# Kernel tuning notes

Measured on AMD Instinct MI355X. Metric: run time of the kernel, lower is better.

Reference implementation:

```python
import jax, jax.numpy as jnp
import numpy as np

THETA = 10000.0
AXES_DIM = (16, 56, 56)  # sums to head_dim=128
HEADS = 24
HEAD_DIM = 128
EPS = 1e-5


def _pos_embed(ids):
    # ids: (S, n_axes) int -> cos, sin each (S, head_dim//2)
    pos = ids.astype(jnp.float32)
    cos_out, sin_out = [], []
    for i, d in enumerate(AXES_DIM):
        freqs = 1.0 / (THETA ** (jnp.arange(0, d, 2, dtype=jnp.float32) / d))  # (d/2,)
        ang = pos[:, i][:, None] * freqs[None, :]  # (S, d/2)
        cos_out.append(jnp.cos(ang))
        sin_out.append(jnp.sin(ang))
    return jnp.concatenate(cos_out, -1), jnp.concatenate(sin_out, -1)


def _rms_norm(x, w):
    # per-head RMSNorm over last dim (head_dim)
    var = jnp.mean(x * x, axis=-1, keepdims=True)
    return x * jax.lax.rsqrt(var + EPS) * w


def _apply_rope(x, cos, sin):
    # non-neox (interleaved) rotary. x: (B,S,H,D), cos/sin: (S,D/2)
    x1 = x[..., 0::2]
    x2 = x[..., 1::2]
    c = cos[None, :, None, :]
    s = sin[None, :, None, :]
    o1 = x1 * c - x2 * s
    o2 = x2 * c + x1 * s
    return jnp.stack([o1, o2], axis=-1).reshape(x.shape)


def setup_inputs() -> dict:
    key = jax.random.key(0)
    ks = jax.random.split(key, 12)
    B, S_img, S_txt, D = 1, 2048, 512, 3072
    sd = 1.0 / np.sqrt(D)
    return {
        "hidden_states": jax.random.normal(ks[0], (B, S_img, D), jnp.float32),
        "encoder_hidden_states": jax.random.normal(ks[1], (B, S_txt, D), jnp.float32),
        "ids": jax.random.randint(ks[2], (S_txt + S_img, 3), 0, 64, jnp.int32),
        "w_qkv": jax.random.normal(ks[3], (D, 3 * D), jnp.float32) * sd,
        "w_add_qkv": jax.random.normal(ks[4], (D, 3 * D), jnp.float32) * sd,
        "b_add_qkv": jax.random.normal(ks[5], (3 * D,), jnp.float32) * 0.02,
        "w_out": jax.random.normal(ks[6], (D, D), jnp.float32) * sd,
        "b_out": jax.random.normal(ks[7], (D,), jnp.float32) * 0.02,
        "w_add_out": jax.random.normal(ks[8], (D, D), jnp.float32) * sd,
        "b_add_out": jax.random.normal(ks[9], (D,), jnp.float32) * 0.02,
        "norm_q_w": jnp.ones((HEAD_DIM,), jnp.float32),
        "norm_k_w": jnp.ones((HEAD_DIM,), jnp.float32),
        "norm_add_q_w": jnp.ones((HEAD_DIM,), jnp.float32),
        "norm_add_k_w": jnp.ones((HEAD_DIM,), jnp.float32),
    }


def reference(hidden_states, encoder_hidden_states, ids, w_qkv, w_add_qkv,
              b_add_qkv, w_out, b_out, w_add_out, b_add_out,
              norm_q_w, norm_k_w, norm_add_q_w, norm_add_k_w):
    B, S_img, D = hidden_states.shape
    S_txt = encoder_hidden_states.shape[1]
    H, Dh = HEADS, HEAD_DIM

    # fused QKV projections
    qkv = hidden_states @ w_qkv  # (B, S_img, 3D)
    q, k, v = jnp.split(qkv, 3, axis=-1)
    q = _rms_norm(q.reshape(B, S_img, H, Dh), norm_q_w)
    k = _rms_norm(k.reshape(B, S_img, H, Dh), norm_k_w)
    v = v.reshape(B, S_img, H, Dh)

    eqkv = encoder_hidden_states @ w_add_qkv + b_add_qkv
    eq, ek, ev = jnp.split(eqkv, 3, axis=-1)
    eq = _rms_norm(eq.reshape(B, S_txt, H, Dh), norm_add_q_w)
    ek = _rms_norm(ek.reshape(B, S_txt, H, Dh), norm_add_k_w)
    ev = ev.reshape(B, S_txt, H, Dh)

    # joint sequence: text first, then image
    q = jnp.concatenate([eq, q], axis=1)
    k = jnp.concatenate([ek, k], axis=1)
    v = jnp.concatenate([ev, v], axis=1)

    # multi-axis RoPE over joint positions
    cos, sin = _pos_embed(ids)  # (S_txt+S_img, Dh/2)
    q = _apply_rope(q, cos, sin)
    k = _apply_rope(k, cos, sin)

    # scaled dot-product attention (non-causal)
    scale = 1.0 / np.sqrt(Dh)
    scores = jnp.einsum("bqhd,bkhd->bhqk", q, k) * scale
    probs = jax.nn.softmax(scores, axis=-1)
    attn = jnp.einsum("bhqk,bkhd->bqhd", probs, v)
    attn = attn.reshape(B, S_txt + S_img, H * Dh)

    enc_out = attn[:, :S_txt] @ w_add_out + b_add_out
    img_out = attn[:, S_txt:] @ w_out + b_out
    return img_out, enc_out
```

## Files before the change

### kernel.cpp

```cpp
#include <hip/hip_runtime.h>

typedef __attribute__((ext_vector_type(8))) short short8;
typedef __attribute__((ext_vector_type(4))) short short4v;
typedef __attribute__((ext_vector_type(4))) float floatx4;

__device__ __forceinline__ float b2f(short b) {
  union { unsigned u; float f; } v; v.u = ((unsigned)(unsigned short)b) << 16; return v.f;
}
__device__ __forceinline__ short f2b(float f) {
  union { float f; unsigned u; } v; v.f = f;
  return (short)((v.u + 0x7fffu + ((v.u >> 16) & 1u)) >> 16);
}
__device__ __forceinline__ unsigned cvtpk(float lo, float hi) {
  unsigned r;
  asm("v_cvt_pk_bf16_f32 %0, %1, %2" : "=v"(r) : "v"(lo), "v"(hi));
  return r;
}
__device__ __forceinline__ float loadf(const void* p, size_t i, bool f32) {
  return f32 ? ((const float*)p)[i] : b2f(((const short*)p)[i]);
}
__device__ __forceinline__ short8 load8(const void* p, size_t i, bool f32) {
  if (f32) {
    const float* fp = (const float*)p + i;
    float4 a = *(const float4*)fp;
    float4 b = *(const float4*)(fp + 4);
    short8 r;
    r[0] = f2b(a.x); r[1] = f2b(a.y); r[2] = f2b(a.z); r[3] = f2b(a.w);
    r[4] = f2b(b.x); r[5] = f2b(b.y); r[6] = f2b(b.z); r[7] = f2b(b.w);
    return r;
  }
  return *(const short8*)((const short*)p + i);
}

__device__ __forceinline__ void gload16(const short* g, short* l) {
  __builtin_amdgcn_global_load_lds(
      (const __attribute__((address_space(1))) unsigned int*)g,
      (__attribute__((address_space(3))) unsigned int*)l, 16, 0, 0);
}

__global__ void detect_dtype(const unsigned short* __restrict__ w, int* __restrict__ flag) {
  __shared__ int cnt;
  if (threadIdx.x == 0) cnt = 0;
  __syncthreads();
  int bad = 0;
  for (int i = threadIdx.x; i < 4096; i += 256) {
    int e = (w[i] >> 7) & 0xFF;
    if (e >= 0xC8) bad++;
  }
  atomicAdd(&cnt, bad);
  __syncthreads();
  if (threadIdx.x == 0) *flag = (cnt > 64) ? 1 : 0;
}

__global__ __launch_bounds__(256)
void cvt_bf16_2(const void* __restrict__ srcA, long n8A,
                const void* __restrict__ srcB, long n8B,
                short* __restrict__ dst, const int* __restrict__ dflag) {
  const bool f32 = (*dflag != 0);
  const long n8 = n8A + n8B;
  long stride = (long)gridDim.x * 256;
  for (long i = (long)blockIdx.x * 256 + threadIdx.x; i < n8; i += stride) {
    const void* s; long e;
    if (i < n8A) { s = srcA; e = i * 8; } else { s = srcB; e = (i - n8A) * 8; }
    if (f32) {
      const float* fp = (const float*)s + e;
      float4 a = *(const float4*)fp;
      float4 b = *(const float4*)(fp + 4);
      short8 r;
      r[0] = f2b(a.x); r[1] = f2b(a.y); r[2] = f2b(a.z); r[3] = f2b(a.w);
      r[4] = f2b(b.x); r[5] = f2b(b.y); r[6] = f2b(b.z); r[7] = f2b(b.w);
      *(short8*)(dst + i * 8) = r;
    } else {
      *(short8*)(dst + i * 8) = *(const short8*)((const short*)s + e);
    }
  }
}

__global__ __launch_bounds__(256)
void cvt_tw(const void* __restrict__ wq, short* __restrict__ wqd,
            const void* __restrict__ waq, short* __restrict__ waqd,
            const void* __restrict__ wo, short* __restrict__ wod,
            const void* __restrict__ wao, short* __restrict__ waod,
            const int* __restrict__ dflag) {
  __shared__ short st[64][72];
  const bool f32 = (*dflag != 0);
  const int K = 3072;
  int b = blockIdx.x;
  const void* src; short* dst; int N, n0, k0;
  if (b < 13824) {
    src = (b < 6912) ? wq : waq;
    dst = (b < 6912) ? wqd : waqd;
    int rem = b % 6912;
    N = 9216; n0 = (rem % 144) << 6; k0 = (rem / 144) << 6;
  } else {
    b -= 13824;
    src = (b < 2304) ? wo : wao;
    dst = (b < 2304) ? wod : waod;
    int rem = b % 2304;
    N = 3072; n0 = (rem % 48) << 6; k0 = (rem / 48) << 6;
  }
  const int c4 = threadIdx.x & 15;
  const int rq = threadIdx.x >> 4;
#pragma unroll
  for (int r = 0; r < 4; ++r) {
    int k = r * 16 + rq;
    int n = c4 * 4;
    short v0, v1, v2, v3;
    if (f32) {
      const float* sp = (const float*)src + (size_t)(k0 + k) * N + n0 + n;
      float4 f = *(const float4*)sp;
      v0 = f2b(f.x); v1 = f2b(f.y); v2 = f2b(f.z); v3 = f2b(f.w);
    } else {
      const short* sp = (const short*)src + (size_t)(k0 + k) * N + n0 + n;
      short4v s = *(const short4v*)sp;
      v0 = s[0]; v1 = s[1]; v2 = s[2]; v3 = s[3];
    }
    st[n + 0][k] = v0; st[n + 1][k] = v1; st[n + 2][k] = v2; st[n + 3][k] = v3;
  }
  __syncthreads();
  const int n = threadIdx.x >> 2;
  const int kc = (threadIdx.x & 3) << 4;
  short8 a = *(const short8*)(&st[n][kc]);
  short8 bb = *(const short8*)(&st[n][kc + 8]);
  short* dp = dst + (size_t)(n0 + n) * K + k0 + kc;
  *(short8*)(dp) = a;
  *(short8*)(dp + 8) = bb;
}

__global__ __launch_bounds__(256, 2)
void gemm_bt(const void* __restrict__ A, int a_row0,
             const void* __restrict__ B, const void* __restrict__ bias,
             void* __restrict__ C, int c_row0, int N, int K,
             const int* __restrict__ dflag, int aIn, int cOut) {
  __shared__ short As[128 * 32];
  __shared__ short Bs[128 * 32];
  const bool f32 = (*dflag != 0);
  const bool a32 = aIn && f32;
  const bool c32 = cOut && f32;
  const int tid = threadIdx.x;
  const int lane = tid & 63, w = tid >> 6;
  const int wm = w & 1, wn = w >> 1;
  const int qg = lane >> 4, l16 = lane & 15;
  const int m0 = blockIdx.y << 7, n0 = blockIdx.x << 7;

  const int arow = tid >> 2, ak = (tid & 3) << 3;
  const int brow = tid >> 4, bc = (tid & 15) << 3;
  const int rot = tid & 15;

  floatx4 acc[4][4];
#pragma unroll
  for (int i = 0; i < 4; ++i)
#pragma unroll
    for (int j = 0; j < 4; ++j) acc[i][j] = (floatx4){0.f, 0.f, 0.f, 0.f};

  for (int k0 = 0; k0 < K; k0 += 32) {
    __syncthreads();
#pragma unroll
    for (int j = 0; j < 2; ++j) {
      short8 av = load8(A, (size_t)(a_row0 + m0 + j * 64 + arow) * K + (k0 + ak), a32);
      *(short8*)(As + (j * 64 + arow) * 32 + ak) = av;
      int kr = j * 16 + brow;
      short8 bv = load8(B, (size_t)(k0 + kr) * N + (n0 + bc), f32);
      int kq = kr >> 3, kj = kr & 7;
#pragma unroll
      for (int s = 0; s < 8; ++s) {
        int u = (s + rot) & 7;
        int n = bc + u;
        Bs[(n << 5) + ((kq ^ (n & 3)) << 3) + kj] = bv[u];
      }
    }
    __syncthreads();
    short8 a[4];
#pragma unroll
    for (int mi = 0; mi < 4; ++mi)
      a[mi] = *(const short8*)(As + (wm * 64 + mi * 16 + l16) * 32 + qg * 8);
#pragma unroll
    for (int ni = 0; ni < 4; ++ni) {
      int n = wn * 64 + ni * 16 + l16;
      short8 b = *(const short8*)(Bs + (n << 5) + ((qg ^ (n & 3)) << 3));
#pragma unroll
      for (int mi = 0; mi < 4; ++mi)
        acc[mi][ni] = __builtin_amdgcn_mfma_f32_16x16x32_bf16(a[mi], b, acc[mi][ni], 0, 0, 0);
    }
  }
#pragma unroll
  for (int ni = 0; ni < 4; ++ni) {
    int col = n0 + wn * 64 + ni * 16 + l16;
    float bv = bias ? loadf(bias, col, f32) : 0.0f;
#pragma unroll
    for (int mi = 0; mi < 4; ++mi) {
      int row = m0 + wm * 64 + mi * 16 + qg * 4;
#pragma unroll
      for (int r = 0; r < 4; ++r) {
        size_t idx = (size_t)(c_row0 + row + r) * N + col;
        float val = acc[mi][ni][r] + bv;
        if (c32) ((float*)C)[idx] = val;
        else     ((short*)C)[idx] = f2b(val);
      }
    }
  }
}

__global__ __launch_bounds__(256, 3)
void gemm_bf2(const short* __restrict__ A,
              const short* __restrict__ BTa, const void* __restrict__ biasa,
              int a0a, int c0a, int nYa,
              const short* __restrict__ BTb, const void* __restrict__ biasb,
              int a0b, int c0b,
              void* __restrict__ C, int N, int K,
              const int* __restrict__ dflag, int cOut) {
  __shared__ short Ls[6 * 128 * 32];
#define ASB(b) (Ls + (b) * 4096)
#define BSB(b) (Ls + (3 + (b)) * 4096)
  const bool f32 = (*dflag != 0);
  const bool c32 = cOut && f32;
  const int bx = blockIdx.x;
  const int y = blockIdx.y;
  const short* BT; const void* bias; int arow0, crow0;
  if (y < nYa) { BT = BTa; bias = biasa; arow0 = a0a + (y << 7); crow0 = c0a + (y << 7); }
  else { int my = y - nYa; BT = BTb; bias = biasb; arow0 = a0b + (my << 7); crow0 = c0b + (my << 7); }
  const int tid = threadIdx.x;
  const int lane = tid & 63, w = tid >> 6;
  const int wm = w & 1, wn = w >> 1;
  const int qg = lane >> 4, l16 = lane & 15;
  const int n0 = bx << 7;
  const int garow = lane >> 2;
  const int gcir = lane & 3;
  const int nk = K >> 5;
  const int swz = (gcir ^ (garow & 3) ^ (garow >> 2)) << 3;
  const short* Abase = A + (size_t)(arow0 + w * 32 + garow) * K + swz;
  const short* Bbase = BT + (size_t)(n0 + w * 32 + garow) * K + swz;
  const int rswz = (l16 & 3) ^ (l16 >> 2);

  floatx4 acc[4][4];
#pragma unroll
  for (int i = 0; i < 4; ++i)
#pragma unroll
    for (int j = 0; j < 4; ++j) acc[i][j] = (floatx4){0.f, 0.f, 0.f, 0.f};

  auto STAGE = [&](int buf, int k0) {
#pragma unroll
    for (int j = 0; j < 2; ++j) {
      gload16(Abase + (size_t)j * 16 * K + k0, ASB(buf) + ((w * 2 + j) << 9));
      gload16(Bbase + (size_t)j * 16 * K + k0, BSB(buf) + ((w * 2 + j) << 9));
    }
  };

  STAGE(0, 0);
  if (nk > 1) STAGE(1, 32);

  int cb = 0;
  for (int t = 0; t < nk; ++t) {
    if (t + 1 < nk) {
      asm volatile("s_waitcnt vmcnt(4) lgkmcnt(0)" ::: "memory");
    } else {
      asm volatile("s_waitcnt vmcnt(0) lgkmcnt(0)" ::: "memory");
    }
    __builtin_amdgcn_s_barrier();
    if (t + 2 < nk) {
      int sb = (cb == 0) ? 2 : cb - 1;
      STAGE(sb, (t + 2) << 5);
    }
    short8 a[4], b[4];
#pragma unroll
    for (int mi = 0; mi < 4; ++mi) {
      int ra = wm * 64 + mi * 16 + l16;
      a[mi] = *(const short8*)(ASB(cb) + (ra << 5) + ((qg ^ rswz) << 3));
    }
#pragma unroll
    for (int ni = 0; ni < 4; ++ni) {
      int n = wn * 64 + ni * 16 + l16;
      b[ni] = *(const short8*)(BSB(cb) + (n << 5) + ((qg ^ rswz) << 3));
    }
    __builtin_amdgcn_s_setprio(1);
#pragma unroll
    for (int ni = 0; ni < 4; ++ni)
#pragma unroll
      for (int mi = 0; mi < 4; ++mi)
        acc[mi][ni] = __builtin_amdgcn_mfma_f32_16x16x32_bf16(a[mi], b[ni], acc[mi][ni], 0, 0, 0);
    __builtin_amdgcn_s_setprio(0);
    cb = (cb == 2) ? 0 : cb + 1;
  }
  __builtin_amdgcn_s_barrier();
  if (!c32) {
    short* wreg = Ls + w * 4096;
#pragma unroll
    for (int ni = 0; ni < 4; ++ni) {
      float bvv = bias ? loadf(bias, n0 + wn * 64 + ni * 16 + l16, f32) : 0.0f;
#pragma unroll
      for (int mi = 0; mi < 4; ++mi)
#pragma unroll
        for (int r = 0; r < 4; ++r)
          wreg[(mi * 16 + qg * 4 + r) * 64 + ni * 16 + l16] = f2b(acc[mi][ni][r] + bvv);
    }
    asm volatile("s_waitcnt lgkmcnt(0)" ::: "memory");
#pragma unroll
    for (int j = 0; j < 8; ++j) {
      int row = j * 8 + (lane >> 3);
      int col = (lane & 7) * 8;
      short8 v = *(const short8*)(wreg + row * 64 + col);
      *(short8*)((short*)C + (size_t)(crow0 + wm * 64 + row) * N + n0 + wn * 64 + col) = v;
    }
  } else {
    float* wregf = (float*)(Ls) + w * 2048;
#pragma unroll
    for (int half = 0; half < 2; ++half) {
#pragma unroll
      for (int nh = 0; nh < 2; ++nh) {
        int ni = half * 2 + nh;
        float bvv = bias ? loadf(bias, n0 + wn * 64 + ni * 16 + l16, f32) : 0.0f;
#pragma unroll
        for (int mi = 0; mi < 4; ++mi)
#pragma unroll
          for (int r = 0; r < 4; ++r)
            wregf[(mi * 16 + qg * 4 + r) * 32 + nh * 16 + l16] = acc[mi][ni][r] + bvv;
      }
      asm volatile("s_waitcnt lgkmcnt(0)" ::: "memory");
#pragma unroll
      for (int j = 0; j < 8; ++j) {
        int row = j * 8 + (lane >> 3);
        int c4 = (lane & 7) * 4;
        float4 v = *(const float4*)(wregf + row * 32 + c4);
        *(float4*)((float*)C + (size_t)(crow0 + wm * 64 + row) * N + n0 + wn * 64 + half * 32 + c4) = v;
      }
      asm volatile("s_waitcnt lgkmcnt(0)" ::: "memory");
    }
  }
#undef ASB
#undef BSB
}

__global__ __launch_bounds__(512)
void norm_rope(short* __restrict__ qkv, const int* __restrict__ ids,
               const void* __restrict__ nqw, const void* __restrict__ nkw,
               const void* __restrict__ naqw, const void* __restrict__ nakw,
               const int* __restrict__ dflag) {
  const bool f32 = (*dflag != 0);
  const int t = blockIdx.x, wv = threadIdx.x >> 6, lane = threadIdx.x & 63;
  const bool txt = t < 512;
  int p = lane, axis; float expo;
  if (p < 8)       { axis = 0; expo = (float)(2 * p) * (1.0f / 16.0f); }
  else if (p < 36) { axis = 1; expo = (float)(2 * (p - 8)) * (1.0f / 56.0f); }
  else             { axis = 2; expo = (float)(2 * (p - 36)) * (1.0f / 56.0f); }
  float freq = __expf(-expo * 9.210340371976184f);
  float ang = (float)ids[t * 3 + axis] * freq;
  float s, c; sincosf(ang, &s, &c);
  const void* qw = txt ? naqw : nqw;
  const void* kw = txt ? nakw : nkw;
  float w0q = loadf(qw, 2 * lane, f32), w1q = loadf(qw, 2 * lane + 1, f32);
  float w0k = loadf(kw, 2 * lane, f32), w1k = loadf(kw, 2 * lane + 1, f32);
  const float QS = 0.08838834764831845f * 1.4426950408889634f;
#pragma unroll
  for (int i = 0; i < 3; ++i) {
    int h = wv + 8 * i;
    short* qp = qkv + (size_t)t * 9216 + h * 128 + 2 * lane;
    short* kp = qp + 3072;
    union { unsigned u; short sh[2]; } qv, kv;
    qv.u = *(const unsigned*)qp;
    kv.u = *(const unsigned*)kp;
    float q0 = b2f(qv.sh[0]), q1 = b2f(qv.sh[1]);
    float k0 = b2f(kv.sh[0]), k1 = b2f(kv.sh[1]);
    float sq = q0 * q0 + q1 * q1, sk = k0 * k0 + k1 * k1;
#pragma unroll
    for (int o = 1; o < 64; o <<= 1) { sq += __shfl_xor(sq, o); sk += __shfl_xor(sk, o); }
    float rq = rsqrtf(sq * (1.0f / 128.0f) + 1e-5f);
    float rk = rsqrtf(sk * (1.0f / 128.0f) + 1e-5f);
    float qn0 = q0 * rq * w0q, qn1 = q1 * rq * w1q;
    float kn0 = k0 * rk * w0k, kn1 = k1 * rk * w1k;
    float qo0 = qn0 * c - qn1 * s, qo1 = qn1 * c + qn0 * s;
    float ko0 = kn0 * c - kn1 * s, ko1 = kn1 * c + kn0 * s;
    union { unsigned u; short sh[2]; } qo, ko;
    qo.sh[0] = f2b(qo0 * QS);
    qo.sh[1] = f2b(qo1 * QS);
    ko.sh[0] = f2b(ko0); ko.sh[1] = f2b(ko1);
    *(unsigned*)qp = qo.u;
    *(unsigned*)kp = ko.u;
  }
}

__global__ __launch_bounds__(512, 2)
void attn_fa(const short* __restrict__ qkv, short* __restrict__ attn) {
  __shared__ short QPs[256 * 128];
  __shared__ short KVs[2][128 * 128];
  const int wgid = blockIdx.x;
  const int xcd = wgid & 7, slot = wgid >> 3;
  const int h = xcd * 3 + slot / 10;
  const int qt = slot % 10;
  const int tid = threadIdx.x, lane = tid & 63, w = tid >> 6;
  const int qg = lane >> 4, l16 = lane & 15;
  const int lr = lane >> 4, lc = lane & 15;
  const int q0 = qt << 8;
  const int sc = tid & 15;
  const int srow5 = (tid >> 4) & 15, half = tid >> 8;

  const short* Qg  = qkv + (size_t)q0 * 9216 + h * 128;
  const short* Kg0 = qkv + 3072 + h * 128;
  const short* Vg0 = qkv + 6144 + h * 128;

  short8 vr[4];
#pragma unroll
  for (int j = 0; j < 8; ++j) {
    int row = j * 32 + w * 4 + lr;
    gload16(Qg + (size_t)row * 9216 + ((lc ^ (row & 7)) << 3),
            QPs + (j * 32 + w * 4) * 128);
  }
#pragma unroll
  for (int j = 0; j < 4; ++j) {
    int row = j * 32 + w * 4 + lr;
    gload16(Kg0 + (size_t)row * 9216 + ((lc ^ (row & 7)) << 3),
            &KVs[0][(j * 32 + w * 4) * 128]);
  }
#pragma unroll
  for (int j = 0; j < 4; ++j) {
    int row = half * 64 + j * 16 + srow5;
    vr[j] = *(const short8*)(Vg0 + (size_t)row * 9216 + sc * 8);
  }
  asm volatile("s_waitcnt vmcnt(8) lgkmcnt(0)" ::: "memory");
  __builtin_amdgcn_s_barrier();
  short8 aq[2][4];
#pragma unroll
  for (int mi = 0; mi < 2; ++mi)
#pragma unroll
    for (int kc = 0; kc < 4; ++kc) {
      int row = w * 32 + mi * 16 + l16;
      aq[mi][kc] = *(const short8*)(QPs + row * 128 + (((kc * 4 + qg) ^ (row & 7)) << 3));
    }

  floatx4 acc_o[2][8];
#pragma unroll
  for (int mi = 0; mi < 2; ++mi)
#pragma unroll
    for (int nd = 0; nd < 8; ++nd) acc_o[mi][nd] = (floatx4){0.f, 0.f, 0.f, 0.f};
  float m_i[2][4], l_i[2][4];
#pragma unroll
  for (int mi = 0; mi < 2; ++mi)
#pragma unroll
    for (int r = 0; r < 4; ++r) { m_i[mi][r] = -1e30f; l_i[mi][r] = 0.0f; }

  for (int kt = 0; kt < 20; ++kt) {
    const int c = kt & 1;
    asm volatile("s_waitcnt vmcnt(4) lgkmcnt(0)" ::: "memory");
    __builtin_amdgcn_s_barrier();
    if (kt < 19) {
      const short* Kg = qkv + ((size_t)(kt + 1) * 128) * 9216 + 3072 + h * 128;
#pragma unroll
      for (int j = 0; j < 4; ++j) {
        int row = j * 32 + w * 4 + lr;
        gload16(Kg + (size_t)row * 9216 + ((lc ^ (row & 7)) << 3),
                &KVs[1 - c][(j * 32 + w * 4) * 128]);
      }
    }
    floatx4 acc_s[2][8];
#pragma unroll
    for (int mi = 0; mi < 2; ++mi)
#pragma unroll
      for (int ni = 0; ni < 8; ++ni) acc_s[mi][ni] = (floatx4){0.f, 0.f, 0.f, 0.f};
    __builtin_amdgcn_s_setprio(1);
#pragma unroll
    for (int kc = 0; kc < 4; ++kc) {
#pragma unroll
      for (int ni = 0; ni < 8; ++ni) {
        int row = ni * 16 + l16;
        short8 b = *(const short8*)(&KVs[c][row * 128 + (((kc * 4 + qg) ^ (row & 7)) << 3)]);
        acc_s[0][ni] = __builtin_amdgcn_mfma_f32_16x16x32_bf16(aq[0][kc], b, acc_s[0][ni], 0, 0, 0);
        acc_s[1][ni] = __builtin_amdgcn_mfma_f32_16x16x32_bf16(aq[1][kc], b, acc_s[1][ni], 0, 0, 0);
      }
    }
    __builtin_amdgcn_s_setprio(0);
    float mxv[2][4];
    bool need = false;
#pragma unroll
    for (int mi = 0; mi < 2; ++mi) {
#pragma unroll
      for (int r = 0; r < 4; ++r) {
        float mx = acc_s[mi][0][r];
#pragma unroll
        for (int ni = 1; ni < 8; ++ni) mx = fmaxf(mx, acc_s[mi][ni][r]);
        mx = fmaxf(mx, __shfl_xor(mx, 1));
        mx = fmaxf(mx, __shfl_xor(mx, 2));
        mx = fmaxf(mx, __shfl_xor(mx, 4));
        mx = fmaxf(mx, __shfl_xor(mx, 8));
        mxv[mi][r] = mx;
        need = need || (mx > m_i[mi][r] + 8.0f);
      }
    }
    if (__ballot(need)) {
#pragma unroll
      for (int mi = 0; mi < 2; ++mi) {
#pragma unroll
        for (int r = 0; r < 4; ++r) {
          float mn = fmaxf(m_i[mi][r], mxv[mi][r]);
          float al = __builtin_amdgcn_exp2f(m_i[mi][r] - mn);
          m_i[mi][r] = mn;
          l_i[mi][r] *= al;
#pragma unroll
          for (int nd = 0; nd < 8; ++nd) acc_o[mi][nd][r] *= al;
        }
      }
    }
#pragma unroll
    for (int mi = 0; mi < 2; ++mi) {
      float rs[4] = {0.f, 0.f, 0.f, 0.f};
#pragma unroll
      for (int r = 0; r < 4; ++r) {
        float pv[8];
#pragma unroll
        for (int ni = 0; ni < 8; ++ni) {
          pv[ni] = __builtin_amdgcn_exp2f(acc_s[mi][ni][r] - m_i[mi][r]);
          rs[r] += pv[ni];
        }
        unsigned u0 = cvtpk(pv[0], pv[1]);
        unsigned u1 = cvtpk(pv[2], pv[3]);
        unsigned u2 = cvtpk(pv[4], pv[5]);
        unsigned u3 = cvtpk(pv[6], pv[7]);
        int row = w * 32 + mi * 16 + qg * 4 + r;
        uint4 uu; uu.x = u0; uu.y = u1; uu.z = u2; uu.w = u3;
        *(uint4*)(QPs + row * 128 + ((l16 ^ (row & 15)) << 3)) = uu;
      }
#pragma unroll
      for (int r = 0; r < 4; ++r) {
        float t = rs[r];
        t += __shfl_xor(t, 1); t += __shfl_xor(t, 2);
        t += __shfl_xor(t, 4); t += __shfl_xor(t, 8);
        l_i[mi][r] += t;
      }
    }
    asm volatile("s_waitcnt lgkmcnt(0)" ::: "memory");
    __builtin_amdgcn_s_barrier();
#pragma unroll
    for (int u = 0; u < 8; ++u) {
      int d = sc * 8 + u;
      short4v pk = { vr[0][u], vr[1][u], vr[2][u], vr[3][u] };
      *(short4v*)(&KVs[c][d * 128 + (((srow5 ^ u ^ (sc & 7))) << 3) + half * 4]) = pk;
    }
    if (kt < 19) {
      const short* Vg = qkv + ((size_t)(kt + 1) * 128) * 9216 + 6144 + h * 128;
#pragma unroll
      for (int j = 0; j < 4; ++j) {
        int row = half * 64 + j * 16 + srow5;
        vr[j] = *(const short8*)(Vg + (size_t)row * 9216 + sc * 8);
      }
    }
    asm volatile("s_waitcnt lgkmcnt(0)" ::: "memory");
    __builtin_amdgcn_s_barrier();
    __builtin_amdgcn_s_setprio(1);
#pragma unroll
    for (int kc = 0; kc < 4; ++kc) {
      int prow0 = w * 32 + l16;
      short8 ap0 = *(const short8*)(QPs + prow0 * 128 + (((kc * 4 + qg) ^ (prow0 & 15)) << 3));
      int prow1 = prow0 + 16;
      short8 ap1 = *(const short8*)(QPs + prow1 * 128 + (((kc * 4 + qg) ^ (prow1 & 15)) << 3));
#pragma unroll
      for (int nd = 0; nd < 8; ++nd) {
        int row = nd * 16 + l16;
        int chn = (kc * 4 + qg) ^ (row & 7) ^ ((row >> 3) & 7);
        short8 b = *(const short8*)(&KVs[c][row * 128 + (chn << 3)]);
        acc_o[0][nd] = __builtin_amdgcn_mfma_f32_16x16x32_bf16(ap0, b, acc_o[0][nd], 0, 0, 0);
        acc_o[1][nd] = __builtin_amdgcn_mfma_f32_16x16x32_bf16(ap1, b, acc_o[1][nd], 0, 0, 0);
      }
    }
    __builtin_amdgcn_s_setprio(0);
  }
#pragma unroll
  for (int mi = 0; mi < 2; ++mi) {
    float inv[4];
#pragma unroll
    for (int r = 0; r < 4; ++r) inv[r] = 1.0f / l_i[mi][r];
#pragma unroll
    for (int nd = 0; nd < 8; ++nd) {
#pragma unroll
      for (int r = 0; r < 4; ++r) {
        int row = w * 32 + mi * 16 + qg * 4 + r;
        QPs[row * 128 + nd * 16 + l16] = f2b(acc_o[mi][nd][r] * inv[r]);
      }
    }
  }
  asm volatile("s_waitcnt lgkmcnt(0)" ::: "memory");
#pragma unroll
  for (int j = 0; j < 8; ++j) {
    int rrow = w * 32 + j * 4 + qg;
    short8 vv = *(const short8*)(QPs + rrow * 128 + l16 * 8);
    *(short8*)(attn + (size_t)(q0 + rrow) * 3072 + h * 128 + l16 * 8) = vv;
  }
}

extern "C" void kernel_launch(void* const* d_in, const int* in_sizes, int n_in,
                              void* d_out, int out_size, void* d_ws, size_t ws_size,
                              hipStream_t stream) {
  (void)in_sizes; (void)n_in; (void)out_size;
  const void* hidden    = d_in[0];
  const void* enc       = d_in[1];
  const int*  ids       = (const int*)d_in[2];
  const void* w_qkv     = d_in[3];
  const void* w_add_qkv = d_in[4];
  const void* b_add_qkv = d_in[5];
  const void* w_out     = d_in[6];
  const void* b_out     = d_in[7];
  const void* w_add_out = d_in[8];
  const void* b_add_out = d_in[9];
  const void* nqw  = d_in[10];
  const void* nkw  = d_in[11];
  const void* naqw = d_in[12];
  const void* nakw = d_in[13];

  int*   dflag = (int*)d_ws;
  short* qkv   = (short*)((char*)d_ws + 256);
  short* attnB = qkv + (size_t)2560 * 9216;

  short* pool  = attnB + (size_t)2560 * 3072;
  const long n_hid  = 2048L * 3072;
  const long n_enc  = 512L * 3072;
  const long n_wqkv = 3072L * 9216;
  const long n_wout = 3072L * 3072;
  short* xb   = pool;
  short* wqb  = xb + n_enc + n_hid;
  short* waqb = wqb + n_wqkv;
  short* wob  = waqb + n_wqkv;
  short* waob = wob + n_wout;
  const size_t REQ = 256 + 2 * ((size_t)2560 * 9216 + (size_t)2560 * 3072 +
                                n_hid + n_enc + 2 * n_wqkv + 2 * n_wout);

  detect_dtype<<<1, 256, 0, stream>>>((const unsigned short*)w_qkv, dflag);

  if (ws_size >= REQ) {
    cvt_bf16_2<<<1024, 256, 0, stream>>>(enc, n_enc / 8, hidden, n_hid / 8, xb, dflag);
    cvt_tw<<<dim3(18432), 256, 0, stream>>>(w_qkv, wqb, w_add_qkv, waqb,
                                            w_out, wob, w_add_out, waob, dflag);

    gemm_bf2<<<dim3(72, 20), 256, 0, stream>>>(
        xb, waqb, b_add_qkv, 0, 0, 4, wqb, nullptr, 512, 512,
        qkv, 9216, 3072, dflag, 0);
    norm_rope<<<dim3(2560), 512, 0, stream>>>(qkv, ids, nqw, nkw, naqw, nakw, dflag);
    attn_fa<<<dim3(240), 512, 0, stream>>>(qkv, attnB);
    gemm_bf2<<<dim3(24, 20), 256, 0, stream>>>(
        attnB, wob, b_out, 512, 0, 16, waob, b_add_out, 0, 2048,
        d_out, 3072, 3072, dflag, 1);
  } else {
    gemm_bt<<<dim3(72, 4), 256, 0, stream>>>(enc, 0, w_add_qkv, b_add_qkv, qkv, 0, 9216, 3072, dflag, 1, 0);
    gemm_bt<<<dim3(72, 16), 256, 0, stream>>>(hidden, 0, w_qkv, nullptr, qkv, 512, 9216, 3072, dflag, 1, 0);
    norm_rope<<<dim3(2560), 512, 0, stream>>>(qkv, ids, nqw, nkw, naqw, nakw, dflag);
    attn_fa<<<dim3(240), 512, 0, stream>>>(qkv, attnB);
    gemm_bt<<<dim3(24, 16), 256, 0, stream>>>(attnB, 512, w_out, b_out, d_out, 0, 3072, 3072, dflag, 0, 1);
    gemm_bt<<<dim3(24, 4), 256, 0, stream>>>(attnB, 0, w_add_out, b_add_out, d_out, 2048, 3072, 3072, dflag, 0, 1);
  }
}
```

Baseline: 792.4 us.

## Enlarge GEMM block tile to 256x128 with 8x4 MFMA per wave

Doubles the M dimension of the gemm_bf2 block tile from 128 to 256 rows, so each wave computes a 128x64 sub-tile with twice the accumulators. Each B tile loaded into shared memory now feeds twice as many MFMAs, which cuts global and LDS traffic per FLOP, and the grid shrinks by half. The cost is more registers and shared memory per block (launch bounds lowered to 2 blocks per CU) and fewer blocks: the output projection drops to 240 blocks, which may not fill all CUs.

After: 792.9 us. No clear change (+0.1%).

```diff
diff --git a/kernel.cpp b/kernel.cpp
--- a/kernel.cpp
+++ b/kernel.cpp
@@ -201,7 +201,7 @@
   }
 }
 
-__global__ __launch_bounds__(256, 3)
+__global__ __launch_bounds__(256, 2)
 void gemm_bf2(const short* __restrict__ A,
               const short* __restrict__ BTa, const void* __restrict__ biasa,
               int a0a, int c0a, int nYa,
@@ -209,16 +209,16 @@
               int a0b, int c0b,
               void* __restrict__ C, int N, int K,
               const int* __restrict__ dflag, int cOut) {
-  __shared__ short Ls[6 * 128 * 32];
-#define ASB(b) (Ls + (b) * 4096)
-#define BSB(b) (Ls + (3 + (b)) * 4096)
+  __shared__ short Ls[3 * 8192 + 3 * 4096];
+#define ASB(b) (Ls + (b) * 8192)
+#define BSB(b) (Ls + 24576 + (b) * 4096)
   const bool f32 = (*dflag != 0);
   const bool c32 = cOut && f32;
   const int bx = blockIdx.x;
   const int y = blockIdx.y;
   const short* BT; const void* bias; int arow0, crow0;
-  if (y < nYa) { BT = BTa; bias = biasa; arow0 = a0a + (y << 7); crow0 = c0a + (y << 7); }
-  else { int my = y - nYa; BT = BTb; bias = biasb; arow0 = a0b + (my << 7); crow0 = c0b + (my << 7); }
+  if (y < nYa) { BT = BTa; bias = biasa; arow0 = a0a + (y << 8); crow0 = c0a + (y << 8); }
+  else { int my = y - nYa; BT = BTb; bias = biasb; arow0 = a0b + (my << 8); crow0 = c0b + (my << 8); }
   const int tid = threadIdx.x;
   const int lane = tid & 63, w = tid >> 6;
   const int wm = w & 1, wn = w >> 1;
@@ -228,22 +228,23 @@
   const int gcir = lane & 3;
   const int nk = K >> 5;
   const int swz = (gcir ^ (garow & 3) ^ (garow >> 2)) << 3;
-  const short* Abase = A + (size_t)(arow0 + w * 32 + garow) * K + swz;
+  const short* Abase = A + (size_t)(arow0 + w * 64 + garow) * K + swz;
   const short* Bbase = BT + (size_t)(n0 + w * 32 + garow) * K + swz;
   const int rswz = (l16 & 3) ^ (l16 >> 2);
 
-  floatx4 acc[4][4];
-#pragma unroll
-  for (int i = 0; i < 4; ++i)
+  floatx4 acc[8][4];
+#pragma unroll
+  for (int i = 0; i < 8; ++i)
 #pragma unroll
     for (int j = 0; j < 4; ++j) acc[i][j] = (floatx4){0.f, 0.f, 0.f, 0.f};
 
   auto STAGE = [&](int buf, int k0) {
 #pragma unroll
-    for (int j = 0; j < 2; ++j) {
-      gload16(Abase + (size_t)j * 16 * K + k0, ASB(buf) + ((w * 2 + j) << 9));
+    for (int j = 0; j < 4; ++j)
+      gload16(Abase + (size_t)j * 16 * K + k0, ASB(buf) + ((w * 4 + j) << 9));
+#pragma unroll
+    for (int j = 0; j < 2; ++j)
       gload16(Bbase + (size_t)j * 16 * K + k0, BSB(buf) + ((w * 2 + j) << 9));
-    }
   };
 
   STAGE(0, 0);
@@ -252,7 +253,7 @@
   int cb = 0;
   for (int t = 0; t < nk; ++t) {
     if (t + 1 < nk) {
-      asm volatile("s_waitcnt vmcnt(4) lgkmcnt(0)" ::: "memory");
+      asm volatile("s_waitcnt vmcnt(6) lgkmcnt(0)" ::: "memory");
     } else {
       asm volatile("s_waitcnt vmcnt(0) lgkmcnt(0)" ::: "memory");
     }
@@ -261,10 +262,10 @@
       int sb = (cb == 0) ? 2 : cb - 1;
       STAGE(sb, (t + 2) << 5);
     }
-    short8 a[4], b[4];
-#pragma unroll
-    for (int mi = 0; mi < 4; ++mi) {
-      int ra = wm * 64 + mi * 16 + l16;
+    short8 a[8], b[4];
+#pragma unroll
+    for (int mi = 0; mi < 8; ++mi) {
+      int ra = wm * 128 + mi * 16 + l16;
       a[mi] = *(const short8*)(ASB(cb) + (ra << 5) + ((qg ^ rswz) << 3));
     }
 #pragma unroll
@@ -276,7 +277,7 @@
 #pragma unroll
     for (int ni = 0; ni < 4; ++ni)
 #pragma unroll
-      for (int mi = 0; mi < 4; ++mi)
+      for (int mi = 0; mi < 8; ++mi)
         acc[mi][ni] = __builtin_amdgcn_mfma_f32_16x16x32_bf16(a[mi], b[ni], acc[mi][ni], 0, 0, 0);
     __builtin_amdgcn_s_setprio(0);
     cb = (cb == 2) ? 0 : cb + 1;
@@ -285,45 +286,56 @@
   if (!c32) {
     short* wreg = Ls + w * 4096;
 #pragma unroll
-    for (int ni = 0; ni < 4; ++ni) {
-      float bvv = bias ? loadf(bias, n0 + wn * 64 + ni * 16 + l16, f32) : 0.0f;
-#pragma unroll
-      for (int mi = 0; mi < 4; ++mi)
-#pragma unroll
-        for (int r = 0; r < 4; ++r)
-          wreg[(mi * 16 + qg * 4 + r) * 64 + ni * 16 + l16] = f2b(acc[mi][ni][r] + bvv);
-    }
-    asm volatile("s_waitcnt lgkmcnt(0)" ::: "memory");
-#pragma unroll
-    for (int j = 0; j < 8; ++j) {
-      int row = j * 8 + (lane >> 3);
-      int col = (lane & 7) * 8;
-      short8 v = *(const short8*)(wreg + row * 64 + col);
-      *(short8*)((short*)C + (size_t)(crow0 + wm * 64 + row) * N + n0 + wn * 64 + col) = v;
+    for (int half = 0; half < 2; ++half) {
+#pragma unroll
+      for (int ni = 0; ni < 4; ++ni) {
+        float bvv = bias ? loadf(bias, n0 + wn * 64 + ni * 16 + l16, f32) : 0.0f;
+#pragma unroll
+        for (int mi2 = 0; mi2 < 4; ++mi2)
+#pragma unroll
+          for (int r = 0; r < 4; ++r)
+            wreg[(mi2 * 16 + qg * 4 + r) * 64 + ni * 16 + l16] =
+                f2b(acc[half * 4 + mi2][ni][r] + bvv);
+      }
+      asm volatile("s_waitcnt lgkmcnt(0)" ::: "memory");
+#pragma unroll
+      for (int j = 0; j < 8; ++j) {
+        int row = j * 8 + (lane >> 3);
+        int col = (lane & 7) * 8;
+        short8 v = *(const short8*)(wreg + row * 64 + col);
+        *(short8*)((short*)C + (size_t)(crow0 + wm * 128 + half * 64 + row) * N +
+                   n0 + wn * 64 + col) = v;
+      }
+      asm volatile("s_waitcnt lgkmcnt(0)" ::: "memory");
     }
   } else {
     float* wregf = (float*)(Ls) + w * 2048;
 #pragma unroll
     for (int half = 0; half < 2; ++half) {
 #pragma unroll
-      for (int nh = 0; nh < 2; ++nh) {
-        int ni = half * 2 + nh;
-        float bvv = bias ? loadf(bias, n0 + wn * 64 + ni * 16 + l16, f32) : 0.0f;
-#pragma unroll
-        for (int mi = 0; mi < 4; ++mi)
-#pragma unroll
-          for (int r = 0; r < 4; ++r)
-            wregf[(mi * 16 + qg * 4 + r) * 32 + nh * 16 + l16] = acc[mi][ni][r] + bvv;
-      }
-      asm volatile("s_waitcnt lgkmcnt(0)" ::: "memory");
-#pragma unroll
-      for (int j = 0; j < 8; ++j) {
-        int row = j * 8 + (lane >> 3);
-        int c4 = (lane & 7) * 4;
-        float4 v = *(const float4*)(wregf + row * 32 + c4);
-        *(float4*)((float*)C + (size_t)(crow0 + wm * 64 + row) * N + n0 + wn * 64 + half * 32 + c4) = v;
-      }
-      asm volatile("s_waitcnt lgkmcnt(0)" ::: "memory");
+      for (int ch = 0; ch < 2; ++ch) {
+#pragma unroll
+        for (int nh = 0; nh < 2; ++nh) {
+          int ni = ch * 2 + nh;
+          float bvv = bias ? loadf(bias, n0 + wn * 64 + ni * 16 + l16, f32) : 0.0f;
+#pragma unroll
+          for (int mi2 = 0; mi2 < 4; ++mi2)
+#pragma unroll
+            for (int r = 0; r < 4; ++r)
+              wregf[(mi2 * 16 + qg * 4 + r) * 32 + nh * 16 + l16] =
+                  acc[half * 4 + mi2][ni][r] + bvv;
+        }
+        asm volatile("s_waitcnt lgkmcnt(0)" ::: "memory");
+#pragma unroll
+        for (int j = 0; j < 8; ++j) {
+          int row = j * 8 + (lane >> 3);
+          int c4 = (lane & 7) * 4;
+          float4 v = *(const float4*)(wregf + row * 32 + c4);
+          *(float4*)((float*)C + (size_t)(crow0 + wm * 128 + half * 64 + row) * N +
+                     n0 + wn * 64 + ch * 32 + c4) = v;
+        }
+        asm volatile("s_waitcnt lgkmcnt(0)" ::: "memory");
+      }
     }
   }
 #undef ASB
@@ -627,13 +639,13 @@
     cvt_tw<<<dim3(18432), 256, 0, stream>>>(w_qkv, wqb, w_add_qkv, waqb,
                                             w_out, wob, w_add_out, waob, dflag);
 
-    gemm_bf2<<<dim3(72, 20), 256, 0, stream>>>(
-        xb, waqb, b_add_qkv, 0, 0, 4, wqb, nullptr, 512, 512,
+    gemm_bf2<<<dim3(72, 10), 256, 0, stream>>>(
+        xb, waqb, b_add_qkv, 0, 0, 2, wqb, nullptr, 512, 512,
         qkv, 9216, 3072, dflag, 0);
     norm_rope<<<dim3(2560), 512, 0, stream>>>(qkv, ids, nqw, nkw, naqw, nakw, dflag);
     attn_fa<<<dim3(240), 512, 0, stream>>>(qkv, attnB);
-    gemm_bf2<<<dim3(24, 20), 256, 0, stream>>>(
-        attnB, wob, b_out, 512, 0, 16, waob, b_add_out, 0, 2048,
+    gemm_bf2<<<dim3(24, 10), 256, 0, stream>>>(
+        attnB, wob, b_out, 512, 0, 8, waob, b_add_out, 0, 2048,
         d_out, 3072, 3072, dflag, 1);
   } else {
     gemm_bt<<<dim3(72, 4), 256, 0, stream>>>(enc, 0, w_add_qkv, b_add_qkv, qkv, 0, 9216, 3072, dflag, 1, 0);
```
